# Kernel optimization log

Measured on AMD Instinct MI355X. Metric: run time of the kernel, lower is better.

## Reference

```python
import jax, jax.numpy as jnp
import numpy as np

N = 200000   # active voxels
G = 128      # dense grid extent per axis
C = 128      # hidden channels
IN_C = 1
TEMB = 6
K = 27       # 3x3x3 kernel offsets


def _build_neighbors():
    # Sample N unique voxel coordinates in a G^3 grid and build the 27-offset
    # rulebook: neighbor_idx[k, i] = index of voxel at coord[i] + offset[k],
    # or N (sentinel -> zero-padded feature row) if inactive.
    rng = np.random.default_rng(0)
    lin = np.sort(rng.choice(G ** 3, size=N, replace=False)).astype(np.int64)
    x, r = lin // (G * G), lin % (G * G)
    y, z = r // G, r % G
    nidx = np.full((K, N), N, dtype=np.int32)
    k = 0
    for dx in (-1, 0, 1):
        for dy in (-1, 0, 1):
            for dz in (-1, 0, 1):
                nx, ny, nz = x + dx, y + dy, z + dz
                valid = (nx >= 0) & (nx < G) & (ny >= 0) & (ny < G) & (nz >= 0) & (nz < G)
                key = nx * (G * G) + ny * G + nz
                pos = np.searchsorted(lin, key)
                posc = np.clip(pos, 0, N - 1)
                found = valid & (lin[posc] == key)
                nidx[k] = np.where(found, posc, N).astype(np.int32)
                k += 1
    return jnp.asarray(nidx)


def setup_inputs() -> dict:
    key = jax.random.key(0)
    ks = jax.random.split(key, 8)
    s = jnp.float32(0.05)
    return {
        "features": jax.random.normal(ks[0], (N, IN_C), jnp.float32),
        "t": jax.random.randint(ks[1], (N,), 0, 1000, jnp.int32),
        "neighbor_idx": _build_neighbors(),
        "W1": jax.random.normal(ks[2], (K, IN_C + TEMB, C), jnp.float32) * s,
        "b1": jnp.zeros((C,), jnp.float32),
        "W2": jax.random.normal(ks[3], (K, C, C), jnp.float32) * s,
        "b2": jnp.zeros((C,), jnp.float32),
        "W3": jax.random.normal(ks[4], (C, C), jnp.float32) * s,
        "b3": jnp.zeros((C,), jnp.float32),
        "W4": jax.random.normal(ks[5], (C, 1), jnp.float32) * s,
        "b4": jnp.zeros((1,), jnp.float32),
    }


def _sinusoidal(t, dim):
    half = dim // 2
    freqs = (2.0 ** jnp.arange(half, dtype=jnp.float32)) * jnp.pi  # 2^k * pi
    ang = t.astype(jnp.float32)[:, None] * freqs[None, :]
    return jnp.concatenate([jnp.sin(ang), jnp.cos(ang)], -1)  # [N, dim]


def _sparse_conv3(x, W, b, nidx):
    # Submanifold sparse 3x3x3 conv: for each of 27 offsets, gather neighbor
    # features (zero row for missing) and accumulate a [Cin,Cout] matmul.
    xpad = jnp.concatenate([x, jnp.zeros((1, x.shape[1]), x.dtype)], 0)  # sentinel row
    acc0 = jnp.zeros((x.shape[0], W.shape[-1]), x.dtype)

    def step(acc, kw):
        idx, Wk = kw
        return acc + xpad[idx] @ Wk, None

    acc, _ = jax.lax.scan(step, acc0, (nidx, W))
    return acc + b


def reference(features, t, neighbor_idx, W1, b1, W2, b2, W3, b3, W4, b4):
    # time-embedding concat  [N, 1+6]
    x = jnp.concatenate([features, _sinusoidal(t, TEMB)], -1)
    # SparseConv3d(k=3) + Dropout(eval: identity) + SiLU
    h = jax.nn.silu(_sparse_conv3(x, W1, b1, neighbor_idx))
    h = jax.nn.silu(_sparse_conv3(h, W2, b2, neighbor_idx))
    # SparseConv3d(k=1) + SiLU  == pointwise matmul
    h = jax.nn.silu(h @ W3 + b3)
    # final 1x1 conv to out_channels=1
    return h @ W4 + b4
```

## Files before the change

kernel.cpp:

```cpp
#include <hip/hip_runtime.h>
#include <math.h>

#define N_VOX 200000
#define CCH   128
#define KOFF  27

typedef __attribute__((ext_vector_type(8))) short bf16x8;
typedef __attribute__((ext_vector_type(4))) float f32x4;

__device__ __forceinline__ float silu_f(float x) {
    return x / (1.0f + expf(-x));
}
__device__ __forceinline__ unsigned short f2bf(float x) {
    unsigned int u = __float_as_uint(x);
    u = (u + 0x7FFFu + ((u >> 16) & 1u)) >> 16;
    return (unsigned short)u;
}
__device__ __forceinline__ int xcd_swz(int orig, int nwg) {
    int q = nwg >> 3, r = nwg & 7;
    int xcd = orig & 7, pos = orig >> 3;
    return (xcd < r ? xcd * (q + 1) : r * (q + 1) + (xcd - r) * q) + pos;
}
__device__ __forceinline__ void gload_lds16(const void* g, void* l) {
    __builtin_amdgcn_global_load_lds(
        (const __attribute__((address_space(1))) unsigned int*)g,
        (__attribute__((address_space(3))) unsigned int*)l, 16, 0, 0);
}

__global__ void embed_kernel(const float* __restrict__ feat,
                             const int* __restrict__ t,
                             unsigned short* __restrict__ xeb) {
    int i = blockIdx.x * blockDim.x + threadIdx.x;
    if (i > N_VOX) return;
    union { unsigned short u[8]; int4 v; } o;
    if (i == N_VOX) {
        o.v = make_int4(0, 0, 0, 0);
    } else {
        o.u[0] = f2bf(feat[i]);
        float tf = (float)t[i];
#pragma unroll
        for (int kk = 0; kk < 3; ++kk) {
            float freq = (float)M_PI * (float)(1 << kk);
            float ang = tf * freq;
            o.u[1 + kk] = f2bf(sinf(ang));
            o.u[4 + kk] = f2bf(cosf(ang));
        }
        o.u[7] = 0;
    }
    *(int4*)(xeb + (size_t)i * 8) = o.v;
}

__global__ void convert_w1(const float* __restrict__ W1,
                           unsigned short* __restrict__ W1f) {
    int g = blockIdx.x * 256 + threadIdx.x;
    if (g >= 7 * 8 * 64) return;
    int l = g & 63;
    int rest = g >> 6;
    int nf = rest & 7;
    int kk = rest >> 3;
    int o = kk * 4 + (l >> 4);
    int co = nf * 16 + (l & 15);
    union { unsigned short u[8]; int4 v; } out;
#pragma unroll
    for (int j = 0; j < 8; ++j) {
        float w = 0.f;
        if (o < KOFF && j < 7) w = W1[((size_t)o * 7 + j) * CCH + co];
        out.u[j] = f2bf(w);
    }
    *(int4*)(W1f + (size_t)g * 8) = out.v;
}

__global__ void convert_w2(const float* __restrict__ W2,
                           unsigned short* __restrict__ W2f) {
    int g = blockIdx.x * 256 + threadIdx.x;
    int l = g & 63;
    int rest = g >> 6;
    int nf = rest & 7;
    int kkk = rest >> 3;
    int k = kkk >> 2, kk = kkk & 3;
    int ci0 = kk * 32 + (l >> 4) * 8;
    int co = nf * 16 + (l & 15);
    union { unsigned short u[8]; int4 v; } out;
#pragma unroll
    for (int j = 0; j < 8; ++j)
        out.u[j] = f2bf(W2[((size_t)k * CCH + ci0 + j) * CCH + co]);
    *(int4*)(W2f + (size_t)g * 8) = out.v;
}

__global__ void convert_w3(const float* __restrict__ W3,
                           unsigned short* __restrict__ W3f) {
    int g = blockIdx.x * 256 + threadIdx.x;
    if (g >= 4 * 8 * 64) return;
    int l = g & 63;
    int rest = g >> 6;
    int nf = rest & 7;
    int kk = rest >> 3;
    int ci0 = kk * 32 + (l >> 4) * 8;
    int co = nf * 16 + (l & 15);
    union { unsigned short u[8]; int4 v; } out;
#pragma unroll
    for (int j = 0; j < 8; ++j)
        out.u[j] = f2bf(W3[(size_t)(ci0 + j) * CCH + co]);
    *(int4*)(W3f + (size_t)g * 8) = out.v;
}

__global__ __launch_bounds__(256) void conv1_mfma(
    const unsigned short* __restrict__ xeb, const int* __restrict__ nidx,
    const unsigned short* __restrict__ W1f, const float* __restrict__ b1,
    unsigned short* __restrict__ h1b) {
    __shared__ int4 bufmem[2048];
    __shared__ int idxAll[128 * 28];

    int tid = threadIdx.x;
    int l = tid & 63, w = tid >> 6;
    int mw = w >> 1, nwv = w & 1;
    int wg = xcd_swz(blockIdx.x, gridDim.x);
    int v0 = wg * 128;

    for (int g = tid; g < KOFF * 128; g += 256) {
        int k = g >> 7, vi = g & 127;
        int v = v0 + vi;
        idxAll[vi * 28 + k] = (v < N_VOX) ? nidx[(size_t)k * N_VOX + v] : N_VOX;
    }
    if (tid < 128) idxAll[tid * 28 + 27] = N_VOX;
    __syncthreads();

    f32x4 acc[4][4];
#pragma unroll
    for (int m = 0; m < 4; ++m)
#pragma unroll
        for (int n = 0; n < 4; ++n) acc[m][n] = (f32x4)0.f;

    {
        int4 g0[2]; int rr[2], cc[2];
#pragma unroll
        for (int u = 0; u < 2; ++u) {
            int q = u * 256 + tid;
            int r = q >> 2, oo = q & 3;
            int idx = idxAll[r * 28 + oo];
            g0[u] = *(const int4*)(xeb + (size_t)idx * 8);
            rr[u] = r; cc[u] = oo ^ (r & 3);
        }
#pragma unroll
        for (int u = 0; u < 2; ++u) bufmem[rr[u] * 5 + cc[u]] = g0[u];
    }
    __syncthreads();

    for (int kk = 0; kk < 7; ++kk) {
        int cur = kk & 1;
        int4 gg[2]; int rr[2], cc[2];
        if (kk < 6) {
#pragma unroll
            for (int u = 0; u < 2; ++u) {
                int q = u * 256 + tid;
                int r = q >> 2, oo = q & 3;
                int idx = idxAll[r * 28 + (kk + 1) * 4 + oo];
                gg[u] = *(const int4*)(xeb + (size_t)idx * 8);
                rr[u] = r; cc[u] = oo ^ (r & 3);
            }
        }
        bf16x8 a[4], b[4];
#pragma unroll
        for (int n = 0; n < 4; ++n) {
            int nf = nwv * 4 + n;
            b[n] = *(const bf16x8*)(W1f + ((size_t)(kk * 8 + nf) * 64 + l) * 8);
        }
#pragma unroll
        for (int m = 0; m < 4; ++m) {
            int r = mw * 64 + m * 16 + (l & 15);
            int c = l >> 4;
            a[m] = *(const bf16x8*)&bufmem[cur * 640 + r * 5 + (c ^ (r & 3))];
        }
#pragma unroll
        for (int m = 0; m < 4; ++m)
#pragma unroll
            for (int n = 0; n < 4; ++n)
                acc[m][n] = __builtin_amdgcn_mfma_f32_16x16x32_bf16(
                    a[m], b[n], acc[m][n], 0, 0, 0);
        if (kk < 6) {
#pragma unroll
            for (int u = 0; u < 2; ++u)
                bufmem[(cur ^ 1) * 640 + rr[u] * 5 + cc[u]] = gg[u];
        }
        __syncthreads();
    }

    float bias[4];
#pragma unroll
    for (int n = 0; n < 4; ++n) bias[n] = b1[nwv * 64 + n * 16 + (l & 15)];
    unsigned short* H16 = (unsigned short*)bufmem;
#pragma unroll
    for (int m = 0; m < 4; ++m) {
        int rbase = mw * 64 + m * 16 + (l >> 4) * 4;
#pragma unroll
        for (int n = 0; n < 4; ++n) {
            int ch = nwv * 64 + n * 16 + (l & 15);
            int c = ch >> 3;
            f32x4 d = acc[m][n];
#pragma unroll
            for (int ri = 0; ri < 4; ++ri) {
                int r = rbase + ri;
                int s = (c & 8) | ((c & 7) ^ (r & 7));
                H16[r * 128 + s * 8 + (ch & 7)] = f2bf(silu_f(d[ri] + bias[n]));
            }
        }
    }
    __syncthreads();
#pragma unroll
    for (int u = 0; u < 8; ++u) {
        int q = u * 256 + tid;
        int r = q >> 4, s = q & 15;
        int c = (s & 8) | ((s & 7) ^ (r & 7));
        int v = v0 + r;
        if (v < N_VOX)
            *(int4*)(h1b + (size_t)v * CCH + c * 8) = bufmem[r * 16 + s];
    }
    if (blockIdx.x == 0 && tid < 16)
        *(int4*)(h1b + (size_t)N_VOX * CCH + tid * 8) = make_int4(0, 0, 0, 0);
}

#define STAGE2(bufsel, kq) {                                               \
    _Pragma("unroll") for (int u = 0; u < 8; ++u) {                        \
        int q = u * 256 + tid;                                             \
        int r = q >> 4, s = q & 15;                                        \
        int c = (s & 8) | ((s & 7) ^ (r & 7));                             \
        int idx = idxAll[(kq) * 128 + r];                                  \
        gload_lds16((const char*)h1b + ((size_t)idx << 8) + (c << 4),      \
                    (void*)&Abuf[bufsel][q]);                              \
    }                                                                      \
}

__global__ __launch_bounds__(256, 2) void conv2_mfma(
    const unsigned short* __restrict__ h1b, const int* __restrict__ nidx,
    const unsigned short* __restrict__ W2f, const float* __restrict__ b2,
    const unsigned short* __restrict__ W3f, const float* __restrict__ b3,
    const float* __restrict__ W4, const float* __restrict__ b4,
    float* __restrict__ out) {
    __shared__ int4 Abuf[2][2048];
    __shared__ int idxAll[KOFF * 128];

    int tid = threadIdx.x;
    int l = tid & 63, w = tid >> 6;
    int mw = w >> 1, nwv = w & 1;
    int wg = xcd_swz(blockIdx.x, gridDim.x);
    int v0 = wg * 128;

    for (int g = tid; g < KOFF * 128; g += 256) {
        int k = g >> 7, vi = g & 127;
        int v = v0 + vi;
        idxAll[k * 128 + vi] = (v < N_VOX) ? nidx[(size_t)k * N_VOX + v] : N_VOX;
    }
    __syncthreads();

    f32x4 acc[4][4];
#pragma unroll
    for (int m = 0; m < 4; ++m)
#pragma unroll
        for (int n = 0; n < 4; ++n) acc[m][n] = (f32x4)0.f;

    STAGE2(0, 0);
    asm volatile("s_waitcnt vmcnt(0)" ::: "memory");
    __builtin_amdgcn_s_barrier();

    for (int k = 0; k < KOFF; ++k) {
        int cur = k & 1;
        const unsigned short* wb = W2f + (size_t)k * 16384;
        bf16x8 bf[4][4];
#pragma unroll
        for (int kk = 0; kk < 4; ++kk)
#pragma unroll
            for (int n = 0; n < 4; ++n)
                bf[kk][n] = *(const bf16x8*)(wb +
                    ((size_t)(kk * 8 + nwv * 4 + n) * 64 + l) * 8);
        __builtin_amdgcn_sched_barrier(0);
        if (k + 1 < KOFF) { STAGE2(cur ^ 1, k + 1); }
        __builtin_amdgcn_sched_barrier(0);
#pragma unroll
        for (int kk = 0; kk < 4; ++kk) {
            bf16x8 a[4];
#pragma unroll
            for (int m = 0; m < 4; ++m) {
                int r = mw * 64 + m * 16 + (l & 15);
                int c = kk * 4 + (l >> 4);
                int s = (c & 8) | ((c & 7) ^ (r & 7));
                a[m] = *(const bf16x8*)&Abuf[cur][r * 16 + s];
            }
#pragma unroll
            for (int m = 0; m < 4; ++m)
#pragma unroll
                for (int n = 0; n < 4; ++n)
                    acc[m][n] = __builtin_amdgcn_mfma_f32_16x16x32_bf16(
                        a[m], bf[kk][n], acc[m][n], 0, 0, 0);
        }
        asm volatile("s_waitcnt vmcnt(0)" ::: "memory");
        __builtin_amdgcn_s_barrier();
    }

    float bias2[4];
#pragma unroll
    for (int n = 0; n < 4; ++n) bias2[n] = b2[nwv * 64 + n * 16 + (l & 15)];
    unsigned short* H16 = (unsigned short*)&Abuf[0][0];
#pragma unroll
    for (int m = 0; m < 4; ++m) {
        int rbase = mw * 64 + m * 16 + (l >> 4) * 4;
#pragma unroll
        for (int n = 0; n < 4; ++n) {
            int ch = nwv * 64 + n * 16 + (l & 15);
            int c = ch >> 3;
            f32x4 d = acc[m][n];
#pragma unroll
            for (int ri = 0; ri < 4; ++ri) {
                int r = rbase + ri;
                int s = (c & 8) | ((c & 7) ^ (r & 7));
                H16[r * 128 + s * 8 + (ch & 7)] = f2bf(silu_f(d[ri] + bias2[n]));
            }
        }
    }
    __syncthreads();

    f32x4 p[4][4];
#pragma unroll
    for (int m = 0; m < 4; ++m)
#pragma unroll
        for (int n = 0; n < 4; ++n) p[m][n] = (f32x4)0.f;
#pragma unroll
    for (int kk = 0; kk < 4; ++kk) {
        bf16x8 a[4], b[4];
#pragma unroll
        for (int n = 0; n < 4; ++n) {
            int nf = nwv * 4 + n;
            b[n] = *(const bf16x8*)(W3f + ((size_t)(kk * 8 + nf) * 64 + l) * 8);
        }
#pragma unroll
        for (int m = 0; m < 4; ++m) {
            int r = mw * 64 + m * 16 + (l & 15);
            int c = kk * 4 + (l >> 4);
            int s = (c & 8) | ((c & 7) ^ (r & 7));
            a[m] = *(const bf16x8*)&H16[r * 128 + s * 8];
        }
#pragma unroll
        for (int m = 0; m < 4; ++m)
#pragma unroll
            for (int n = 0; n < 4; ++n)
                p[m][n] = __builtin_amdgcn_mfma_f32_16x16x32_bf16(
                    a[m], b[n], p[m][n], 0, 0, 0);
    }

    float w4v[4], b3v[4];
#pragma unroll
    for (int n = 0; n < 4; ++n) {
        int ch = nwv * 64 + n * 16 + (l & 15);
        w4v[n] = W4[ch];
        b3v[n] = b3[ch];
    }
    float* Osum = (float*)idxAll;
#pragma unroll
    for (int m = 0; m < 4; ++m) {
        float po[4] = {0.f, 0.f, 0.f, 0.f};
#pragma unroll
        for (int n = 0; n < 4; ++n) {
            f32x4 d = p[m][n];
#pragma unroll
            for (int ri = 0; ri < 4; ++ri)
                po[ri] += silu_f(d[ri] + b3v[n]) * w4v[n];
        }
#pragma unroll
        for (int off = 1; off < 16; off <<= 1)
#pragma unroll
            for (int ri = 0; ri < 4; ++ri)
                po[ri] += __shfl_xor(po[ri], off, 64);
        if ((l & 15) == 0) {
            int rbase = mw * 64 + m * 16 + (l >> 4) * 4;
#pragma unroll
            for (int ri = 0; ri < 4; ++ri)
                Osum[nwv * 128 + rbase + ri] = po[ri];
        }
    }
    __syncthreads();
    if (tid < 128) {
        int v = v0 + tid;
        if (v < N_VOX) out[v] = Osum[tid] + Osum[128 + tid] + b4[0];
    }
}

extern "C" void kernel_launch(void* const* d_in, const int* in_sizes, int n_in,
                              void* d_out, int out_size, void* d_ws,
                              size_t ws_size, hipStream_t stream) {
    const float* feat = (const float*)d_in[0];
    const int* t      = (const int*)d_in[1];
    const int* nidx   = (const int*)d_in[2];
    const float* W1   = (const float*)d_in[3];
    const float* b1   = (const float*)d_in[4];
    const float* W2   = (const float*)d_in[5];
    const float* b2   = (const float*)d_in[6];
    const float* W3   = (const float*)d_in[7];
    const float* b3   = (const float*)d_in[8];
    const float* W4   = (const float*)d_in[9];
    const float* b4   = (const float*)d_in[10];
    float* out = (float*)d_out;

    char* ws = (char*)d_ws;
    size_t off = 0;
    unsigned short* xeb = (unsigned short*)(ws + off);
    off += ((size_t)(N_VOX + 1) * 8 * 2 + 255) & ~(size_t)255;
    unsigned short* h1b = (unsigned short*)(ws + off);
    off += ((size_t)(N_VOX + 1) * CCH * 2 + 255) & ~(size_t)255;
    unsigned short* W1f = (unsigned short*)(ws + off);
    off += ((size_t)7 * 8 * 64 * 8 * 2 + 255) & ~(size_t)255;
    unsigned short* W2f = (unsigned short*)(ws + off);
    off += ((size_t)KOFF * 4 * 8 * 64 * 8 * 2 + 255) & ~(size_t)255;
    unsigned short* W3f = (unsigned short*)(ws + off);

    int grid1 = (N_VOX + 127) / 128;
    int grid2 = (N_VOX + 127) / 128;
    embed_kernel<<<(N_VOX + 1 + 255) / 256, 256, 0, stream>>>(feat, t, xeb);
    convert_w1<<<(7 * 8 * 64 + 255) / 256, 256, 0, stream>>>(W1, W1f);
    convert_w2<<<(KOFF * 4 * 8 * 64) / 256, 256, 0, stream>>>(W2, W2f);
    convert_w3<<<(4 * 8 * 64 + 255) / 256, 256, 0, stream>>>(W3, W3f);
    conv1_mfma<<<grid1, 256, 0, stream>>>(xeb, nidx, W1f, b1, h1b);
    conv2_mfma<<<grid2, 256, 0, stream>>>(h1b, nidx, W2f, b2, W3f, b3, W4, b4, out);
}
```

Measured before the change: 296.5 us.

## Interleave gather and weight loads with MFMA phases in conv2 main loop

The conv2 k-loop is split into four kk phases. Each phase issues a quarter of the next offset's LDS gather plus the next B-fragment register load, then runs its MFMAs on the current data. B fragments are double-buffered in two register sets instead of all 16 being loaded up front, and the wait drops to vmcnt(4) so the prefetched B loads stay in flight across the barrier. s_setprio raises priority around the MFMA bursts. This is meant to hide gather and weight-load latency behind matrix math and to cut register pressure, at the cost of a manually peeled last iteration and careful vmcnt accounting.

New measurement: 355.3 us. 1.2x slower.

```diff
diff --git a/kernel.cpp b/kernel.cpp
--- a/kernel.cpp
+++ b/kernel.cpp
@@ -219,15 +219,38 @@
         *(int4*)(h1b + (size_t)N_VOX * CCH + tid * 8) = make_int4(0, 0, 0, 0);
 }
 
-#define STAGE2(bufsel, kq) {                                               \
-    _Pragma("unroll") for (int u = 0; u < 8; ++u) {                        \
-        int q = u * 256 + tid;                                             \
+#define SPART(bufsel, kq, ph) {                                            \
+    _Pragma("unroll") for (int uu = 0; uu < 2; ++uu) {                     \
+        int q = ((ph) * 2 + uu) * 256 + tid;                               \
         int r = q >> 4, s = q & 15;                                        \
         int c = (s & 8) | ((s & 7) ^ (r & 7));                             \
         int idx = idxAll[(kq) * 128 + r];                                  \
         gload_lds16((const char*)h1b + ((size_t)idx << 8) + (c << 4),      \
                     (void*)&Abuf[bufsel][q]);                              \
     }                                                                      \
+}
+
+#define LOADB(dst, kq, kk) {                                               \
+    const unsigned short* _wb = W2f + (size_t)(kq) * 16384;                \
+    _Pragma("unroll") for (int n = 0; n < 4; ++n)                          \
+        dst[n] = *(const bf16x8*)(_wb +                                    \
+            ((size_t)((kk) * 8 + nwv * 4 + n) * 64 + l) * 8);              \
+}
+
+#define MPHASE(cur, kk, breg) {                                            \
+    bf16x8 _a[4];                                                          \
+    _Pragma("unroll") for (int m = 0; m < 4; ++m) {                        \
+        int r = mw * 64 + m * 16 + (l & 15);                               \
+        int c = (kk) * 4 + (l >> 4);                                       \
+        int s = (c & 8) | ((c & 7) ^ (r & 7));                             \
+        _a[m] = *(const bf16x8*)&Abuf[cur][r * 16 + s];                    \
+    }                                                                      \
+    __builtin_amdgcn_s_setprio(1);                                         \
+    _Pragma("unroll") for (int m = 0; m < 4; ++m)                          \
+        _Pragma("unroll") for (int n = 0; n < 4; ++n)                      \
+            acc[m][n] = __builtin_amdgcn_mfma_f32_16x16x32_bf16(           \
+                _a[m], breg[n], acc[m][n], 0, 0, 0);                       \
+    __builtin_amdgcn_s_setprio(0);                                         \
 }
 
 __global__ __launch_bounds__(256, 2) void conv2_mfma(
@@ -258,43 +281,49 @@
 #pragma unroll
         for (int n = 0; n < 4; ++n) acc[m][n] = (f32x4)0.f;
 
-    STAGE2(0, 0);
-    asm volatile("s_waitcnt vmcnt(0)" ::: "memory");
+    bf16x8 bX[4], bY[4];
+
+    SPART(0, 0, 0); SPART(0, 0, 1); SPART(0, 0, 2); SPART(0, 0, 3);
+    __builtin_amdgcn_sched_barrier(0);
+    LOADB(bX, 0, 0);
+    __builtin_amdgcn_sched_barrier(0);
+    asm volatile("s_waitcnt vmcnt(4)" ::: "memory");
     __builtin_amdgcn_s_barrier();
 
-    for (int k = 0; k < KOFF; ++k) {
-        int cur = k & 1;
-        const unsigned short* wb = W2f + (size_t)k * 16384;
-        bf16x8 bf[4][4];
-#pragma unroll
-        for (int kk = 0; kk < 4; ++kk)
-#pragma unroll
-            for (int n = 0; n < 4; ++n)
-                bf[kk][n] = *(const bf16x8*)(wb +
-                    ((size_t)(kk * 8 + nwv * 4 + n) * 64 + l) * 8);
-        __builtin_amdgcn_sched_barrier(0);
-        if (k + 1 < KOFF) { STAGE2(cur ^ 1, k + 1); }
-        __builtin_amdgcn_sched_barrier(0);
-#pragma unroll
-        for (int kk = 0; kk < 4; ++kk) {
-            bf16x8 a[4];
-#pragma unroll
-            for (int m = 0; m < 4; ++m) {
-                int r = mw * 64 + m * 16 + (l & 15);
-                int c = kk * 4 + (l >> 4);
-                int s = (c & 8) | ((c & 7) ^ (r & 7));
-                a[m] = *(const bf16x8*)&Abuf[cur][r * 16 + s];
-            }
-#pragma unroll
-            for (int m = 0; m < 4; ++m)
-#pragma unroll
-                for (int n = 0; n < 4; ++n)
-                    acc[m][n] = __builtin_amdgcn_mfma_f32_16x16x32_bf16(
-                        a[m], bf[kk][n], acc[m][n], 0, 0, 0);
-        }
-        asm volatile("s_waitcnt vmcnt(0)" ::: "memory");
+    for (int k = 0; k < 26; ++k) {
+        int cur = k & 1, nxt = cur ^ 1;
+        LOADB(bY, k, 1);
+        SPART(nxt, k + 1, 0);
+        __builtin_amdgcn_sched_barrier(0);
+        MPHASE(cur, 0, bX);
+        __builtin_amdgcn_sched_barrier(0);
+        LOADB(bX, k, 2);
+        SPART(nxt, k + 1, 1);
+        __builtin_amdgcn_sched_barrier(0);
+        MPHASE(cur, 1, bY);
+        __builtin_amdgcn_sched_barrier(0);
+        LOADB(bY, k, 3);
+        SPART(nxt, k + 1, 2);
+        __builtin_amdgcn_sched_barrier(0);
+        MPHASE(cur, 2, bX);
+        __builtin_amdgcn_sched_barrier(0);
+        SPART(nxt, k + 1, 3);
+        __builtin_amdgcn_sched_barrier(0);
+        LOADB(bX, k + 1, 0);
+        __builtin_amdgcn_sched_barrier(0);
+        MPHASE(cur, 3, bY);
+        asm volatile("s_waitcnt vmcnt(4)" ::: "memory");
         __builtin_amdgcn_s_barrier();
     }
+    LOADB(bY, 26, 1);
+    MPHASE(0, 0, bX);
+    LOADB(bX, 26, 2);
+    MPHASE(0, 1, bY);
+    LOADB(bY, 26, 3);
+    MPHASE(0, 2, bX);
+    MPHASE(0, 3, bY);
+
+    __syncthreads();
 
     float bias2[4];
 #pragma unroll
```

## Pipeline conv2 weight loads across offsets and use an MFMA-native LDS layout

Applied to the files above, without the earlier changes.

The conv2 main loop is restructured into a two-offset unrolled pipeline. Half of each offset's W2 fragments are prefetched into registers one iteration ahead, and the wait before the barrier is relaxed from vmcnt(0) to vmcnt(8) so those weight loads can stay in flight across it. The gathered activation tile is now staged in LDS in the exact per-lane order the MFMA reads it, which removes the XOR swizzle arithmetic on the read side. The cost is less contiguous global gathers, since each lane group now covers 16 different rows per chunk, plus higher register pressure from the double-buffered weight fragments.

Measured after the change: 303.4 us. 2.3% more time.

```diff
diff --git a/kernel.cpp b/kernel.cpp
--- a/kernel.cpp
+++ b/kernel.cpp
@@ -219,15 +219,49 @@
         *(int4*)(h1b + (size_t)N_VOX * CCH + tid * 8) = make_int4(0, 0, 0, 0);
 }
 
-#define STAGE2(bufsel, kq) {                                               \
-    _Pragma("unroll") for (int u = 0; u < 8; ++u) {                        \
-        int q = u * 256 + tid;                                             \
-        int r = q >> 4, s = q & 15;                                        \
-        int c = (s & 8) | ((s & 7) ^ (r & 7));                             \
-        int idx = idxAll[(kq) * 128 + r];                                  \
-        gload_lds16((const char*)h1b + ((size_t)idx << 8) + (c << 4),      \
-                    (void*)&Abuf[bufsel][q]);                              \
+#define STAGE3(bufsel, kq) {                                               \
+    int _c = (w << 2) + (l >> 4);                                          \
+    _Pragma("unroll") for (int _u = 0; _u < 8; ++_u) {                     \
+        int _r = _u * 16 + (l & 15);                                       \
+        int _idx = idxAll[(kq) * 128 + _r];                                \
+        gload_lds16((const char*)h1b + ((size_t)_idx << 8) + (_c << 4),    \
+                    (void*)&Abuf[bufsel][_u * 256 + tid]);                 \
     }                                                                      \
+}
+
+#define LOADB2(dst, kq, kh) {                                              \
+    const unsigned short* _wb = W2f + (size_t)(kq) * 16384;                \
+    _Pragma("unroll") for (int _j = 0; _j < 2; ++_j)                       \
+        _Pragma("unroll") for (int _n = 0; _n < 4; ++_n)                   \
+            dst[_j][_n] = *(const bf16x8*)(_wb +                           \
+                ((size_t)(((kh)*2 + _j) * 8 + nwv * 4 + _n) * 64 + l) * 8);\
+}
+
+#define MPH(cur, kk, br) {                                                 \
+    bf16x8 _a[4];                                                          \
+    _Pragma("unroll") for (int _m = 0; _m < 4; ++_m)                       \
+        _a[_m] = *(const bf16x8*)                                          \
+            &Abuf[cur][(((mw * 4 + _m) * 4 + (kk)) << 6) + l];             \
+    _Pragma("unroll") for (int _m = 0; _m < 4; ++_m)                       \
+        _Pragma("unroll") for (int _n = 0; _n < 4; ++_n)                   \
+            acc[_m][_n] = __builtin_amdgcn_mfma_f32_16x16x32_bf16(         \
+                _a[_m], br[_n], acc[_m][_n], 0, 0, 0);                     \
+}
+
+#define STEP(KQ, BCUR, BNXT) {                                             \
+    int _cur = (KQ) & 1, _nxt = _cur ^ 1;                                  \
+    STAGE3(_nxt, (KQ) + 1);                                                \
+    __builtin_amdgcn_sched_barrier(0);                                     \
+    bf16x8 b23[2][4];                                                      \
+    LOADB2(b23, (KQ), 1);                                                  \
+    LOADB2(BNXT, (KQ) + 1, 0);                                             \
+    __builtin_amdgcn_sched_barrier(0);                                     \
+    MPH(_cur, 0, BCUR[0]);                                                 \
+    MPH(_cur, 1, BCUR[1]);                                                 \
+    MPH(_cur, 2, b23[0]);                                                  \
+    MPH(_cur, 3, b23[1]);                                                  \
+    asm volatile("s_waitcnt vmcnt(8)" ::: "memory");                       \
+    __builtin_amdgcn_s_barrier();                                          \
 }
 
 __global__ __launch_bounds__(256, 2) void conv2_mfma(
@@ -258,43 +292,28 @@
 #pragma unroll
         for (int n = 0; n < 4; ++n) acc[m][n] = (f32x4)0.f;
 
-    STAGE2(0, 0);
-    asm volatile("s_waitcnt vmcnt(0)" ::: "memory");
+    bf16x8 bE[2][4], bO[2][4];
+
+    STAGE3(0, 0);
+    __builtin_amdgcn_sched_barrier(0);
+    LOADB2(bE, 0, 0);
+    __builtin_amdgcn_sched_barrier(0);
+    asm volatile("s_waitcnt vmcnt(8)" ::: "memory");
     __builtin_amdgcn_s_barrier();
 
-    for (int k = 0; k < KOFF; ++k) {
-        int cur = k & 1;
-        const unsigned short* wb = W2f + (size_t)k * 16384;
-        bf16x8 bf[4][4];
-#pragma unroll
-        for (int kk = 0; kk < 4; ++kk)
-#pragma unroll
-            for (int n = 0; n < 4; ++n)
-                bf[kk][n] = *(const bf16x8*)(wb +
-                    ((size_t)(kk * 8 + nwv * 4 + n) * 64 + l) * 8);
-        __builtin_amdgcn_sched_barrier(0);
-        if (k + 1 < KOFF) { STAGE2(cur ^ 1, k + 1); }
-        __builtin_amdgcn_sched_barrier(0);
-#pragma unroll
-        for (int kk = 0; kk < 4; ++kk) {
-            bf16x8 a[4];
-#pragma unroll
-            for (int m = 0; m < 4; ++m) {
-                int r = mw * 64 + m * 16 + (l & 15);
-                int c = kk * 4 + (l >> 4);
-                int s = (c & 8) | ((c & 7) ^ (r & 7));
-                a[m] = *(const bf16x8*)&Abuf[cur][r * 16 + s];
-            }
-#pragma unroll
-            for (int m = 0; m < 4; ++m)
-#pragma unroll
-                for (int n = 0; n < 4; ++n)
-                    acc[m][n] = __builtin_amdgcn_mfma_f32_16x16x32_bf16(
-                        a[m], bf[kk][n], acc[m][n], 0, 0, 0);
-        }
-        asm volatile("s_waitcnt vmcnt(0)" ::: "memory");
-        __builtin_amdgcn_s_barrier();
-    }
+    for (int kp = 0; kp < 26; kp += 2) {
+        STEP(kp, bE, bO);
+        STEP(kp + 1, bO, bE);
+    }
+    {
+        bf16x8 b23[2][4];
+        LOADB2(b23, 26, 1);
+        MPH(0, 0, bE[0]);
+        MPH(0, 1, bE[1]);
+        MPH(0, 2, b23[0]);
+        MPH(0, 3, b23[1]);
+    }
+    __syncthreads();
 
     float bias2[4];
 #pragma unroll
```

## Split conv2 K-loop into half-channel steps with triple-buffered LDS pipeline

Applied to the files above, without the earlier changes.

The conv2 main loop now iterates over 54 half-K steps of 64 input channels each, using three LDS buffers instead of two. The gather for the next step is issued while MFMAs run on the current one, and partial vmcnt waits replace the full drain. Neighbor indices are pre-transposed in LDS so each lane reads four indices with one int4 load. Weight fragments are double-buffered in registers, and MFMA sections are wrapped in setprio. The aim is to hide gather latency and shorten barrier stalls. The trade-offs are higher register and LDS pressure and extra padding, since the loop reads one dummy offset past the last weight slab, which the enlarged workspace covers.

Result: slower. 311.7 us (+5.1%).

```diff
diff --git a/kernel.cpp b/kernel.cpp
--- a/kernel.cpp
+++ b/kernel.cpp
@@ -4,6 +4,7 @@
 #define N_VOX 200000
 #define CCH   128
 #define KOFF  27
+#define NSTEPS 54
 
 typedef __attribute__((ext_vector_type(8))) short bf16x8;
 typedef __attribute__((ext_vector_type(4))) float f32x4;
@@ -219,15 +220,38 @@
         *(int4*)(h1b + (size_t)N_VOX * CCH + tid * 8) = make_int4(0, 0, 0, 0);
 }
 
-#define STAGE2(bufsel, kq) {                                               \
-    _Pragma("unroll") for (int u = 0; u < 8; ++u) {                        \
-        int q = u * 256 + tid;                                             \
-        int r = q >> 4, s = q & 15;                                        \
-        int c = (s & 8) | ((s & 7) ^ (r & 7));                             \
-        int idx = idxAll[(kq) * 128 + r];                                  \
-        gload_lds16((const char*)h1b + ((size_t)idx << 8) + (c << 4),      \
-                    (void*)&Abuf[bufsel][q]);                              \
-    }                                                                      \
+#define STAGE1(dst, kh, IDX, U) {                                          \
+    gload_lds16((const char*)h1b + ((size_t)(unsigned)(IDX) << 8) +        \
+                    ((kh) << 7) + ((w & 1) << 6) + (hi << 4),              \
+                (void*)&(dst)[((U) * 4 + w) * 64 + l]);                    \
+}
+#define STAGE4(dst, kh, i4) {                                              \
+    STAGE1(dst, kh, (i4).x, 0); STAGE1(dst, kh, (i4).y, 1);                \
+    STAGE1(dst, kh, (i4).z, 2); STAGE1(dst, kh, (i4).w, 3);                \
+}
+
+#define LOADB8(dst, stp) {                                                 \
+    const unsigned short* _wb = W2f +                                      \
+        (size_t)(((stp) >> 1) * 4 + ((stp) & 1) * 2) * 4096;               \
+    _Pragma("unroll") for (int _kk = 0; _kk < 2; ++_kk)                    \
+        _Pragma("unroll") for (int _n = 0; _n < 4; ++_n)                   \
+            dst[_kk][_n] = *(const bf16x8*)(_wb +                          \
+                ((size_t)(_kk * 8 + nwv * 4 + _n) * 64 + l) * 8);          \
+}
+
+#define COMPUTE(src, br) {                                                 \
+    bf16x8 _a[2][4];                                                       \
+    _Pragma("unroll") for (int _kk = 0; _kk < 2; ++_kk)                    \
+        _Pragma("unroll") for (int _m = 0; _m < 4; ++_m)                   \
+            _a[_kk][_m] = *(const bf16x8*)                                 \
+                &(src)[(((mw * 4 + _m) * 2 + _kk) << 6) + l];              \
+    __builtin_amdgcn_s_setprio(1);                                         \
+    _Pragma("unroll") for (int _kk = 0; _kk < 2; ++_kk)                    \
+        _Pragma("unroll") for (int _m = 0; _m < 4; ++_m)                   \
+            _Pragma("unroll") for (int _n = 0; _n < 4; ++_n)               \
+                acc[_m][_n] = __builtin_amdgcn_mfma_f32_16x16x32_bf16(     \
+                    _a[_kk][_m], br[_kk][_n], acc[_m][_n], 0, 0, 0);       \
+    __builtin_amdgcn_s_setprio(0);                                         \
 }
 
 __global__ __launch_bounds__(256, 2) void conv2_mfma(
@@ -236,19 +260,22 @@
     const unsigned short* __restrict__ W3f, const float* __restrict__ b3,
     const float* __restrict__ W4, const float* __restrict__ b4,
     float* __restrict__ out) {
-    __shared__ int4 Abuf[2][2048];
-    __shared__ int idxAll[KOFF * 128];
+    __shared__ int4 Abuf[3 * 1024];
+    __shared__ int idxT[16 * 2 * 29 * 4];
 
     int tid = threadIdx.x;
     int l = tid & 63, w = tid >> 6;
     int mw = w >> 1, nwv = w & 1;
+    int lo = l & 15, hi = l >> 4;
     int wg = xcd_swz(blockIdx.x, gridDim.x);
     int v0 = wg * 128;
 
-    for (int g = tid; g < KOFF * 128; g += 256) {
+    for (int g = tid; g < 28 * 128; g += 256) {
         int k = g >> 7, vi = g & 127;
+        int lo_ = vi & 15, grp = vi >> 4;
         int v = v0 + vi;
-        idxAll[k * 128 + vi] = (v < N_VOX) ? nidx[(size_t)k * N_VOX + v] : N_VOX;
+        idxT[((lo_ * 2 + (grp & 1)) * 29 + k) * 4 + (grp >> 1)] =
+            (k < KOFF && v < N_VOX) ? nidx[(size_t)k * N_VOX + v] : N_VOX;
     }
     __syncthreads();
 
@@ -258,48 +285,49 @@
 #pragma unroll
         for (int n = 0; n < 4; ++n) acc[m][n] = (f32x4)0.f;
 
-    STAGE2(0, 0);
+    const int* myidx = &idxT[(lo * 2 + mw) * 29 * 4];
+    bf16x8 bX[2][4], bY[2][4];
+    int4* P0 = &Abuf[0];
+    int4* P1 = &Abuf[1024];
+    int4* P2 = &Abuf[2048];
+
+    int4 i4cur = *(const int4*)&myidx[0];
+    STAGE4(P0, 0, i4cur);
+    __builtin_amdgcn_sched_barrier(0);
+    LOADB8(bX, 0);
+    __builtin_amdgcn_sched_barrier(0);
+    STAGE4(P1, 1, i4cur);
+    __builtin_amdgcn_sched_barrier(0);
+    i4cur = *(const int4*)&myidx[4];
+
+    for (int tp = 0; tp < NSTEPS; tp += 2) {
+        int k2 = (tp >> 1) + 1;
+        int kn = (k2 + 1 < 28) ? k2 + 1 : 27;
+        asm volatile("s_waitcnt vmcnt(4)" ::: "memory");
+        __builtin_amdgcn_s_barrier();
+        int4 i4next = *(const int4*)&myidx[kn * 4];
+        LOADB8(bY, tp + 1);
+        __builtin_amdgcn_sched_barrier(0);
+        STAGE4(P2, 0, i4cur);
+        __builtin_amdgcn_sched_barrier(0);
+        COMPUTE(P0, bX);
+        asm volatile("s_waitcnt vmcnt(4)" ::: "memory");
+        __builtin_amdgcn_s_barrier();
+        LOADB8(bX, tp + 2);
+        __builtin_amdgcn_sched_barrier(0);
+        STAGE4(P0, 1, i4cur);
+        __builtin_amdgcn_sched_barrier(0);
+        COMPUTE(P1, bY);
+        int4* tmp = P0; P0 = P2; P2 = P1; P1 = tmp;
+        i4cur = i4next;
+    }
     asm volatile("s_waitcnt vmcnt(0)" ::: "memory");
-    __builtin_amdgcn_s_barrier();
-
-    for (int k = 0; k < KOFF; ++k) {
-        int cur = k & 1;
-        const unsigned short* wb = W2f + (size_t)k * 16384;
-        bf16x8 bf[4][4];
-#pragma unroll
-        for (int kk = 0; kk < 4; ++kk)
-#pragma unroll
-            for (int n = 0; n < 4; ++n)
-                bf[kk][n] = *(const bf16x8*)(wb +
-                    ((size_t)(kk * 8 + nwv * 4 + n) * 64 + l) * 8);
-        __builtin_amdgcn_sched_barrier(0);
-        if (k + 1 < KOFF) { STAGE2(cur ^ 1, k + 1); }
-        __builtin_amdgcn_sched_barrier(0);
-#pragma unroll
-        for (int kk = 0; kk < 4; ++kk) {
-            bf16x8 a[4];
-#pragma unroll
-            for (int m = 0; m < 4; ++m) {
-                int r = mw * 64 + m * 16 + (l & 15);
-                int c = kk * 4 + (l >> 4);
-                int s = (c & 8) | ((c & 7) ^ (r & 7));
-                a[m] = *(const bf16x8*)&Abuf[cur][r * 16 + s];
-            }
-#pragma unroll
-            for (int m = 0; m < 4; ++m)
-#pragma unroll
-                for (int n = 0; n < 4; ++n)
-                    acc[m][n] = __builtin_amdgcn_mfma_f32_16x16x32_bf16(
-                        a[m], bf[kk][n], acc[m][n], 0, 0, 0);
-        }
-        asm volatile("s_waitcnt vmcnt(0)" ::: "memory");
-        __builtin_amdgcn_s_barrier();
-    }
+    __syncthreads();
 
     float bias2[4];
 #pragma unroll
     for (int n = 0; n < 4; ++n) bias2[n] = b2[nwv * 64 + n * 16 + (l & 15)];
-    unsigned short* H16 = (unsigned short*)&Abuf[0][0];
+    unsigned short* H16 = (unsigned short*)&Abuf[0];
 #pragma unroll
     for (int m = 0; m < 4; ++m) {
         int rbase = mw * 64 + m * 16 + (l >> 4) * 4;
@@ -353,7 +381,7 @@
         w4v[n] = W4[ch];
         b3v[n] = b3[ch];
     }
-    float* Osum = (float*)idxAll;
+    float* Osum = (float*)idxT;
 #pragma unroll
     for (int m = 0; m < 4; ++m) {
         float po[4] = {0.f, 0.f, 0.f, 0.f};
@@ -408,7 +436,7 @@
     unsigned short* W1f = (unsigned short*)(ws + off);
     off += ((size_t)7 * 8 * 64 * 8 * 2 + 255) & ~(size_t)255;
     unsigned short* W2f = (unsigned short*)(ws + off);
-    off += ((size_t)KOFF * 4 * 8 * 64 * 8 * 2 + 255) & ~(size_t)255;
+    off += ((size_t)(KOFF + 1) * 4 * 8 * 64 * 8 * 2 + 255) & ~(size_t)255;
     unsigned short* W3f = (unsigned short*)(ws + off);
 
     int grid1 = (N_VOX + 127) / 128;
```
